# Kernel optimization log

Hardware: AMD Instinct MI355X
Metric: run time of the kernel (lower is better)

The kernel has to match this reference:

```python
import jax, jax.numpy as jnp
import numpy as np

E = 128    # embedding_size
N = 8192   # total vertices (64 graphs x 128)
CN = 512   # total color slots
G = 64     # number of graphs
TMAX = 32


def _mlp3(x, W, b):
    # 3-layer MLP: Linear-ReLU-Linear-ReLU-Linear. W: [3,E,E], b: [3,E]
    h = jax.nn.relu(x @ W[0].T + b[0])
    h = jax.nn.relu(h @ W[1].T + b[1])
    return h @ W[2].T + b[2]


def _lstm_cell(x, h, c, Wih, Whh, bih, bhh):
    # PyTorch LSTM gate order: i, f, g, o
    gates = x @ Wih.T + h @ Whh.T + (bih + bhh)
    i, f, g, o = jnp.split(gates, 4, axis=-1)
    c2 = jax.nn.sigmoid(f) * c + jax.nn.sigmoid(i) * jnp.tanh(g)
    h2 = jax.nn.sigmoid(o) * jnp.tanh(c2)
    return h2, c2


def setup_inputs() -> dict:
    key = jax.random.key(0)
    ks = jax.random.split(key, 24)
    s = 1.0 / np.sqrt(E)
    f32 = jnp.float32
    inp = {
        "M_vv": jax.random.normal(ks[0], (N, N), f32) * s,
        "M_vc": jax.random.uniform(ks[1], (N, CN), f32) * (1.0 / np.sqrt(CN)),
        "C": jax.random.normal(ks[2], (CN, E), f32),
        "slice_idx": jnp.full((G,), N // G, dtype=jnp.int32),
        "v_emb_w": jax.random.normal(ks[3], (E, 1), f32) * s,
        "v_emb_b": jax.random.normal(ks[4], (E,), f32) * s,
        "mlpC_W": jax.random.normal(ks[5], (3, E, E), f32) * s,
        "mlpC_b": jax.random.normal(ks[6], (3, E), f32) * s,
        "mlpV_W": jax.random.normal(ks[7], (3, E, E), f32) * s,
        "mlpV_b": jax.random.normal(ks[8], (3, E), f32) * s,
        "Wih_v": jax.random.normal(ks[9], (4 * E, 2 * E), f32) * s,
        "Whh_v": jax.random.normal(ks[10], (4 * E, E), f32) * s,
        "bih_v": jax.random.normal(ks[11], (4 * E,), f32) * s,
        "bhh_v": jax.random.normal(ks[12], (4 * E,), f32) * s,
        "Wih_c": jax.random.normal(ks[13], (4 * E, E), f32) * s,
        "Whh_c": jax.random.normal(ks[14], (4 * E, E), f32) * s,
        "bih_c": jax.random.normal(ks[15], (4 * E,), f32) * s,
        "bhh_c": jax.random.normal(ks[16], (4 * E,), f32) * s,
        "vote_W1": jax.random.normal(ks[17], (E, E), f32) * s,
        "vote_b1": jax.random.normal(ks[18], (E,), f32) * s,
        "vote_W2": jax.random.normal(ks[19], (E, E), f32) * s,
        "vote_b2": jax.random.normal(ks[20], (E,), f32) * s,
        "vote_W3": jax.random.normal(ks[21], (1, E), f32) * s,
        "vote_b3": jax.random.normal(ks[22], (1,), f32) * s,
    }
    return inp


def reference(M_vv, M_vc, C, slice_idx, v_emb_w, v_emb_b, mlpC_W, mlpC_b,
              mlpV_W, mlpV_b, Wih_v, Whh_v, bih_v, bhh_v, Wih_c, Whh_c,
              bih_c, bhh_c, vote_W1, vote_b1, vote_W2, vote_b2, vote_W3, vote_b3):
    n = M_vv.shape[0]
    g = slice_idx.shape[0]
    # V = v_emb(ones(1)) broadcast to all vertices: [N, E]
    v0 = v_emb_w[:, 0] + v_emb_b
    V = jnp.broadcast_to(v0, (n, E))
    # Original torch loop never reassigns V, so both LSTM inputs are
    # loop-invariant; compute them once (identical math, no recompute).
    x_v = jnp.concatenate([M_vv @ V, M_vc @ _mlp3(C, mlpC_W, mlpC_b)], axis=1)  # [N, 2E]
    x_c = M_vc.T @ _mlp3(V, mlpV_W, mlpV_b)                                      # [CN, E]

    def step(carry, _):
        hv, cv, hc, cc = carry
        hv, cv = _lstm_cell(x_v, hv, cv, Wih_v, Whh_v, bih_v, bhh_v)
        hc, cc = _lstm_cell(x_c, hc, cc, Wih_c, Whh_c, bih_c, bhh_c)
        return (hv, cv, hc, cc), None

    init = (V, jnp.zeros_like(V), C, jnp.zeros_like(C))
    (hv, cv, hc, cc), _ = jax.lax.scan(step, init, None, length=TMAX)

    # vote MLP on final vertex hidden state -> [N, 1]
    h = jax.nn.relu(hv @ vote_W1.T + vote_b1)
    h = jax.nn.relu(h @ vote_W2.T + vote_b2)
    v_vote = (h @ vote_W3.T + vote_b3)[:, 0]  # [N]

    # per-graph mean then sigmoid (torch: split + mean + sigmoid + vstack)
    seg = jnp.repeat(jnp.arange(g), slice_idx, total_repeat_length=n)
    sums = jax.ops.segment_sum(v_vote, seg, num_segments=g)
    ret = jax.nn.sigmoid(sums / slice_idx.astype(sums.dtype))
    return (ret, V[None], C)
```

## Files before the change

### kernel.cpp

```cpp
#include <hip/hip_runtime.h>
#include <hip/hip_bf16.h>
#include <stdint.h>


typedef __bf16 bf16x8 __attribute__((ext_vector_type(8)));
typedef float f32x4 __attribute__((ext_vector_type(4)));

#define EDIM 128
#define NVERT 8192
#define CNUM 512
#define NG 64
#define TSTEPS 32

#define WS_RS 0u
#define WS_V0 32768u
#define WS_W1 33280u
#define WS_BV 35328u
#define WS_ACC 37376u
#define WS_V0BF 37632u
#define WS_MLPC3T 38912u

__device__ __forceinline__ float bf2f(unsigned short s) {
  return __uint_as_float(((unsigned)s) << 16);
}
__device__ __forceinline__ unsigned short f2bf(float f) {
  unsigned u = __float_as_uint(f);
  u += 0x7fffu + ((u >> 16) & 1u);
  return (unsigned short)(u >> 16);
}
__device__ __forceinline__ float sigm(float x) {
  return __builtin_amdgcn_rcpf(1.f + __expf(-x));
}
__device__ __forceinline__ float tanh_f(float x) {
  return 1.f - 2.f * __builtin_amdgcn_rcpf(1.f + __expf(2.f * x));
}
__device__ __forceinline__ f32x4 mfma16(bf16x8 a, bf16x8 b, f32x4 c) {
  return __builtin_amdgcn_mfma_f32_16x16x32_bf16(a, b, c, 0, 0, 0);
}
__device__ __forceinline__ bf16x8 ld8(const float* p) {
  float4 a = *(const float4*)p;
  float4 b = *(const float4*)(p + 4);
  bf16x8 r;
  r[0] = (__bf16)a.x; r[1] = (__bf16)a.y; r[2] = (__bf16)a.z; r[3] = (__bf16)a.w;
  r[4] = (__bf16)b.x; r[5] = (__bf16)b.y; r[6] = (__bf16)b.z; r[7] = (__bf16)b.w;
  return r;
}

__global__ __launch_bounds__(256) void k_rowsum(
    const float* __restrict__ M, const float* __restrict__ v0,
    float* __restrict__ rs, float* __restrict__ Vout) {
  const int row = blockIdx.x;
  const float4* p = (const float4*)(M + (size_t)row * NVERT);
  float s = 0.f;
#pragma unroll
  for (int it = 0; it < 8; it++) {
    float4 q = p[it * 256 + threadIdx.x];
    s += q.x + q.y + q.z + q.w;
  }
  if (threadIdx.x < 32)
    ((float4*)(Vout + (size_t)row * EDIM))[threadIdx.x] =
        ((const float4*)v0)[threadIdx.x];
#pragma unroll
  for (int off = 32; off > 0; off >>= 1) s += __shfl_down(s, off, 64);
  __shared__ float red[4];
  if ((threadIdx.x & 63) == 0) red[threadIdx.x >> 6] = s;
  __syncthreads();
  if (threadIdx.x == 0) rs[row] = red[0] + red[1] + red[2] + red[3];
}

__global__ __launch_bounds__(512) void k_prep(
    const float* __restrict__ vw, const float* __restrict__ vb,
    const float* __restrict__ Wih,
    const float* __restrict__ bih, const float* __restrict__ bhh,
    float* __restrict__ ws) {
  __shared__ float v0s[EDIM];
  const int t = threadIdx.x;
  float* v0 = (float*)((char*)ws + WS_V0);
  float* w1 = (float*)((char*)ws + WS_W1);
  float* bv = (float*)((char*)ws + WS_BV);
  float* acc = (float*)((char*)ws + WS_ACC);
  unsigned short* v0bf = (unsigned short*)((char*)ws + WS_V0BF);
  if (t < EDIM) {
    float v = vw[t] + vb[t];
    v0s[t] = v;
    v0[t] = v;
    v0bf[t] = f2bf(v);
  }
  if (t < NG) acc[t] = 0.f;
  __syncthreads();
  {
    const float4* wr = (const float4*)(Wih + (size_t)t * 256);
    float s = 0.f;
#pragma unroll
    for (int kc = 0; kc < 32; kc++) {
      float4 q = wr[kc];
      const float* xi = v0s + kc * 4;
      s += q.x * xi[0] + q.y * xi[1] + q.z * xi[2] + q.w * xi[3];
    }
    w1[t] = s;
    bv[t] = bih[t] + bhh[t];
  }
}

__global__ __launch_bounds__(128) void k_mlpc(
    const float* __restrict__ C, const float* __restrict__ W,
    const float* __restrict__ B, float* __restrict__ ws,
    float* __restrict__ Cout) {
  unsigned short* out_t = (unsigned short*)((char*)ws + WS_MLPC3T);
  const int c = blockIdx.x, e = threadIdx.x;
  __shared__ float xb[2][EDIM];
  float cval = C[c * EDIM + e];
  xb[0][e] = cval;
  Cout[c * EDIM + e] = cval;
  __syncthreads();
#pragma unroll
  for (int l = 0; l < 3; l++) {
    const float4* wrow = (const float4*)(W + ((size_t)l * EDIM + e) * EDIM);
    const float* xin = xb[l & 1];
    float s = B[l * EDIM + e];
#pragma unroll
    for (int kc = 0; kc < EDIM / 4; kc++) {
      float4 q = wrow[kc];
      const float* xi = xin + kc * 4;
      s += q.x * xi[0] + q.y * xi[1] + q.z * xi[2] + q.w * xi[3];
    }
    if (l < 2) {
      s = fmaxf(s, 0.f);
      __syncthreads();
      xb[(l + 1) & 1][e] = s;
      __syncthreads();
    } else {
      out_t[(size_t)e * CNUM + c] = f2bf(s);
    }
  }
}

__global__ __launch_bounds__(512, 1) void k_lstm(
    const float* __restrict__ Mvc, const float* __restrict__ Wih,
    const float* __restrict__ Whh,
    const float* __restrict__ W1, const float* __restrict__ b1,
    const float* __restrict__ W2, const float* __restrict__ b2,
    const float* __restrict__ W3, const float* __restrict__ b3,
    float* __restrict__ ws) {
  const int r0 = blockIdx.x * 32;
  const int t = threadIdx.x;
  const int w = t >> 6;
  const int lane = t & 63;
  const int quad = lane >> 4;
  const int l15 = lane & 15;
  const int nc0 = w * 16;

  __shared__ unsigned short Avc[32][CNUM + 8];
  __shared__ unsigned short Tt[32][EDIM + 8];
  __shared__ unsigned short hv2[2][32][EDIM + 8];
  __shared__ float votes[32];

  const float* rs = (const float*)((const char*)ws + WS_RS);
  const float* w1v = (const float*)((const char*)ws + WS_W1);
  const float* bvv = (const float*)((const char*)ws + WS_BV);
  float* accg = (float*)((char*)ws + WS_ACC);
  const unsigned short* v0bf = (const unsigned short*)((const char*)ws + WS_V0BF);
  const unsigned short* m3t = (const unsigned short*)((const char*)ws + WS_MLPC3T);

  {
    const int row = t >> 4, c0 = t & 15;
    const float4* g = (const float4*)(Mvc + (size_t)(r0 + row) * CNUM);
#pragma unroll
    for (int it = 0; it < 8; it++) {
      int c4 = it * 16 + c0;
      float4 q = g[c4];
      ushort4 h;
      h.x = f2bf(q.x); h.y = f2bf(q.y); h.z = f2bf(q.z); h.w = f2bf(q.w);
      *(ushort4*)&Avc[row][c4 * 4] = h;
    }
  }
  for (int i = t; i < 32 * EDIM; i += 512) hv2[0][i >> 7][i & 127] = v0bf[i & 127];
  __syncthreads();

  {
    f32x4 acc[2];
#pragma unroll
    for (int mt = 0; mt < 2; mt++) {
      acc[mt][0] = 0.f; acc[mt][1] = 0.f; acc[mt][2] = 0.f; acc[mt][3] = 0.f;
    }
#pragma unroll
    for (int kc = 0; kc < 16; kc++) {
      bf16x8 a0 = *(const bf16x8*)&Avc[l15][kc * 32 + quad * 8];
      bf16x8 a1 = *(const bf16x8*)&Avc[16 + l15][kc * 32 + quad * 8];
      bf16x8 b0 = *(const bf16x8*)&m3t[(size_t)(nc0 + l15) * CNUM + kc * 32 + quad * 8];
      acc[0] = mfma16(a0, b0, acc[0]);
      acc[1] = mfma16(a1, b0, acc[1]);
    }
#pragma unroll
    for (int mt = 0; mt < 2; mt++)
#pragma unroll
      for (int r = 0; r < 4; r++)
        Tt[mt * 16 + quad * 4 + r][nc0 + l15] = f2bf(acc[mt][r]);
  }
  __syncthreads();

  f32x4 xg[2][4];
  {
    float rsv[2][4];
#pragma unroll
    for (int mt = 0; mt < 2; mt++)
#pragma unroll
      for (int r = 0; r < 4; r++) rsv[mt][r] = rs[r0 + mt * 16 + quad * 4 + r];
#pragma unroll
    for (int gi = 0; gi < 4; gi++) {
      const int col = gi * 128 + nc0 + l15;
      const float w1c = w1v[col], bvc = bvv[col];
#pragma unroll
      for (int mt = 0; mt < 2; mt++)
#pragma unroll
        for (int r = 0; r < 4; r++) xg[mt][gi][r] = fmaf(rsv[mt][r], w1c, bvc);
    }
#pragma unroll
    for (int kc = 0; kc < 4; kc++) {
      bf16x8 a0 = *(const bf16x8*)&Tt[l15][kc * 32 + quad * 8];
      bf16x8 a1 = *(const bf16x8*)&Tt[16 + l15][kc * 32 + quad * 8];
#pragma unroll
      for (int gi = 0; gi < 4; gi++) {
        const int gcol = gi * 128 + nc0 + l15;
        bf16x8 bfr = ld8(&Wih[(size_t)gcol * 256 + 128 + kc * 32 + quad * 8]);
        xg[0][gi] = mfma16(a0, bfr, xg[0][gi]);
        xg[1][gi] = mfma16(a1, bfr, xg[1][gi]);
      }
    }
  }

  bf16x8 Bh[4][4];
#pragma unroll
  for (int gi = 0; gi < 4; gi++) {
    const int gcol = gi * 128 + nc0 + l15;
#pragma unroll
    for (int kc = 0; kc < 4; kc++)
      Bh[gi][kc] = ld8(&Whh[(size_t)gcol * EDIM + kc * 32 + quad * 8]);
  }

  f32x4 cv[2];
#pragma unroll
  for (int mt = 0; mt < 2; mt++) {
    cv[mt][0] = 0.f; cv[mt][1] = 0.f; cv[mt][2] = 0.f; cv[mt][3] = 0.f;
  }

  int p = 0;
#pragma unroll 1
  for (int step = 0; step < TSTEPS; step++) {
    bf16x8 A[2][4];
#pragma unroll
    for (int mt = 0; mt < 2; mt++)
#pragma unroll
      for (int kc = 0; kc < 4; kc++)
        A[mt][kc] = *(const bf16x8*)&hv2[p][mt * 16 + l15][kc * 32 + quad * 8];
#pragma unroll
    for (int mt = 0; mt < 2; mt++) {
      f32x4 gI = xg[mt][0], gF = xg[mt][1], gG = xg[mt][2], gO = xg[mt][3];
#pragma unroll
      for (int kc = 0; kc < 4; kc++) {
        gI = mfma16(A[mt][kc], Bh[0][kc], gI);
        gF = mfma16(A[mt][kc], Bh[1][kc], gF);
        gG = mfma16(A[mt][kc], Bh[2][kc], gG);
        gO = mfma16(A[mt][kc], Bh[3][kc], gO);
      }
#pragma unroll
      for (int r = 0; r < 4; r++) {
        float ig = sigm(gI[r]), fg = sigm(gF[r]);
        float gg = tanh_f(gG[r]), og = sigm(gO[r]);
        float c2 = fmaf(fg, cv[mt][r], ig * gg);
        cv[mt][r] = c2;
        hv2[p ^ 1][mt * 16 + quad * 4 + r][nc0 + l15] = f2bf(og * tanh_f(c2));
      }
    }
    p ^= 1;
    __syncthreads();
  }

  for (int layer = 0; layer < 2; layer++) {
    const float* Wg = layer ? W2 : W1;
    const float* bg = layer ? b2 : b1;
    bf16x8 A[2][4];
#pragma unroll
    for (int mt = 0; mt < 2; mt++)
#pragma unroll
      for (int kc = 0; kc < 4; kc++)
        A[mt][kc] = *(const bf16x8*)&hv2[0][mt * 16 + l15][kc * 32 + quad * 8];
    f32x4 acc[2];
    {
      float bb = bg[nc0 + l15];
#pragma unroll
      for (int mt = 0; mt < 2; mt++) {
        acc[mt][0] = bb; acc[mt][1] = bb; acc[mt][2] = bb; acc[mt][3] = bb;
      }
    }
#pragma unroll
    for (int kc = 0; kc < 4; kc++) {
      bf16x8 bfr = ld8(&Wg[(size_t)(nc0 + l15) * EDIM + kc * 32 + quad * 8]);
      acc[0] = mfma16(A[0][kc], bfr, acc[0]);
      acc[1] = mfma16(A[1][kc], bfr, acc[1]);
    }
    __syncthreads();
#pragma unroll
    for (int mt = 0; mt < 2; mt++)
#pragma unroll
      for (int r = 0; r < 4; r++)
        hv2[0][mt * 16 + quad * 4 + r][nc0 + l15] = f2bf(fmaxf(acc[mt][r], 0.f));
    __syncthreads();
  }

  {
    const int row = t >> 4, seg = t & 15;
    float part = 0.f;
#pragma unroll
    for (int j = 0; j < 8; j++) {
      const int k = seg * 8 + j;
      part += bf2f(hv2[0][row][k]) * W3[k];
    }
    part += __shfl_down(part, 8, 16);
    part += __shfl_down(part, 4, 16);
    part += __shfl_down(part, 2, 16);
    part += __shfl_down(part, 1, 16);
    if (seg == 0) votes[row] = part + b3[0];
    __syncthreads();
    if (t < 64) {
      float v = (t < 32) ? votes[t] : 0.f;
#pragma unroll
      for (int off = 32; off > 0; off >>= 1) v += __shfl_down(v, off, 64);
      if (t == 0) atomicAdd(&accg[blockIdx.x >> 2], v);
    }
  }
}

__global__ __launch_bounds__(64) void k_final(const float* __restrict__ ws,
                                              const int* __restrict__ slice,
                                              float* __restrict__ out) {
  const float* accg = (const float*)((const char*)ws + WS_ACC);
  const int g = threadIdx.x;
  float m = accg[g] / (float)slice[g];
  out[g] = 1.f / (1.f + __expf(-m));
}

extern "C" void kernel_launch(void* const* d_in, const int* in_sizes, int n_in,
                              void* d_out, int out_size, void* d_ws, size_t ws_size,
                              hipStream_t stream) {
  const float* M_vv = (const float*)d_in[0];
  const float* M_vc = (const float*)d_in[1];
  const float* C = (const float*)d_in[2];
  const int* slice = (const int*)d_in[3];
  const float* vw = (const float*)d_in[4];
  const float* vb = (const float*)d_in[5];
  const float* mW = (const float*)d_in[6];
  const float* mB = (const float*)d_in[7];
  const float* Wih = (const float*)d_in[10];
  const float* Whh = (const float*)d_in[11];
  const float* bih = (const float*)d_in[12];
  const float* bhh = (const float*)d_in[13];
  const float* W1 = (const float*)d_in[18];
  const float* b1 = (const float*)d_in[19];
  const float* W2 = (const float*)d_in[20];
  const float* b2 = (const float*)d_in[21];
  const float* W3 = (const float*)d_in[22];
  const float* b3 = (const float*)d_in[23];
  float* ws = (float*)d_ws;
  float* out = (float*)d_out;

  k_prep<<<1, 512, 0, stream>>>(vw, vb, Wih, bih, bhh, ws);
  k_rowsum<<<NVERT, 256, 0, stream>>>(M_vv, (const float*)((char*)ws + WS_V0),
                                      (float*)((char*)ws + WS_RS), out + NG);
  k_mlpc<<<CNUM, 128, 0, stream>>>(C, mW, mB, ws, out + NG + NVERT * EDIM);
  k_lstm<<<256, 512, 0, stream>>>(M_vc, Wih, Whh, W1, b1, W2, b2, W3, b3, ws);
  k_final<<<1, 64, 0, stream>>>(ws, slice, out);
}
```

Before: 511.8 us.

## Fuse rowsum, prep and final kernels into setup and main kernels

Merges the prep kernel into the C-MLP kernel as an extra block, folds the M_vv row-sum and V output copy into the LSTM kernel, and replaces the final sigmoid kernel with a last-block-done atomic counter. This cuts the launch count from five to two and removes the separate row-sum kernel. The trade-off is that the 256MB M_vv read now runs across only 256 blocks of 512 threads at one block per CU, which may give lower memory-level parallelism than the old 8192-block row-sum kernel.

```diff
diff --git a/kernel.cpp b/kernel.cpp
--- a/kernel.cpp
+++ b/kernel.cpp
@@ -12,7 +12,7 @@
 #define NG 64
 #define TSTEPS 32
 
-#define WS_RS 0u
+#define WS_CNT 0u
 #define WS_V0 32768u
 #define WS_W1 33280u
 #define WS_BV 35328u
@@ -46,69 +46,48 @@
   return r;
 }
 
-__global__ __launch_bounds__(256) void k_rowsum(
-    const float* __restrict__ M, const float* __restrict__ v0,
-    float* __restrict__ rs, float* __restrict__ Vout) {
-  const int row = blockIdx.x;
-  const float4* p = (const float4*)(M + (size_t)row * NVERT);
-  float s = 0.f;
-#pragma unroll
-  for (int it = 0; it < 8; it++) {
-    float4 q = p[it * 256 + threadIdx.x];
-    s += q.x + q.y + q.z + q.w;
-  }
-  if (threadIdx.x < 32)
-    ((float4*)(Vout + (size_t)row * EDIM))[threadIdx.x] =
-        ((const float4*)v0)[threadIdx.x];
-#pragma unroll
-  for (int off = 32; off > 0; off >>= 1) s += __shfl_down(s, off, 64);
-  __shared__ float red[4];
-  if ((threadIdx.x & 63) == 0) red[threadIdx.x >> 6] = s;
-  __syncthreads();
-  if (threadIdx.x == 0) rs[row] = red[0] + red[1] + red[2] + red[3];
-}
-
-__global__ __launch_bounds__(512) void k_prep(
-    const float* __restrict__ vw, const float* __restrict__ vb,
-    const float* __restrict__ Wih,
+__global__ __launch_bounds__(128) void k_setup(
+    const float* __restrict__ C, const float* __restrict__ W,
+    const float* __restrict__ B, const float* __restrict__ vw,
+    const float* __restrict__ vb, const float* __restrict__ Wih,
     const float* __restrict__ bih, const float* __restrict__ bhh,
-    float* __restrict__ ws) {
-  __shared__ float v0s[EDIM];
+    float* __restrict__ ws, float* __restrict__ Cout) {
+  __shared__ float xb[2][EDIM];
   const int t = threadIdx.x;
-  float* v0 = (float*)((char*)ws + WS_V0);
-  float* w1 = (float*)((char*)ws + WS_W1);
-  float* bv = (float*)((char*)ws + WS_BV);
-  float* acc = (float*)((char*)ws + WS_ACC);
-  unsigned short* v0bf = (unsigned short*)((char*)ws + WS_V0BF);
-  if (t < EDIM) {
+
+  if (blockIdx.x == CNUM) {
+    float* v0 = (float*)((char*)ws + WS_V0);
+    float* w1 = (float*)((char*)ws + WS_W1);
+    float* bvp = (float*)((char*)ws + WS_BV);
+    float* acc = (float*)((char*)ws + WS_ACC);
+    unsigned short* v0bf = (unsigned short*)((char*)ws + WS_V0BF);
+    unsigned int* cnt = (unsigned int*)((char*)ws + WS_CNT);
     float v = vw[t] + vb[t];
-    v0s[t] = v;
+    xb[0][t] = v;
     v0[t] = v;
     v0bf[t] = f2bf(v);
-  }
-  if (t < NG) acc[t] = 0.f;
-  __syncthreads();
-  {
-    const float4* wr = (const float4*)(Wih + (size_t)t * 256);
-    float s = 0.f;
-#pragma unroll
-    for (int kc = 0; kc < 32; kc++) {
-      float4 q = wr[kc];
-      const float* xi = v0s + kc * 4;
-      s += q.x * xi[0] + q.y * xi[1] + q.z * xi[2] + q.w * xi[3];
-    }
-    w1[t] = s;
-    bv[t] = bih[t] + bhh[t];
-  }
-}
-
-__global__ __launch_bounds__(128) void k_mlpc(
-    const float* __restrict__ C, const float* __restrict__ W,
-    const float* __restrict__ B, float* __restrict__ ws,
-    float* __restrict__ Cout) {
+    if (t < NG) acc[t] = 0.f;
+    if (t == 0) *cnt = 0u;
+    __syncthreads();
+#pragma unroll
+    for (int gi = 0; gi < 4; gi++) {
+      const int col = gi * EDIM + t;
+      const float4* wr = (const float4*)(Wih + (size_t)col * 256);
+      float s = 0.f;
+#pragma unroll
+      for (int kc = 0; kc < 32; kc++) {
+        float4 q = wr[kc];
+        const float* xi = xb[0] + kc * 4;
+        s += q.x * xi[0] + q.y * xi[1] + q.z * xi[2] + q.w * xi[3];
+      }
+      w1[col] = s;
+      bvp[col] = bih[col] + bhh[col];
+    }
+    return;
+  }
+
   unsigned short* out_t = (unsigned short*)((char*)ws + WS_MLPC3T);
-  const int c = blockIdx.x, e = threadIdx.x;
-  __shared__ float xb[2][EDIM];
+  const int c = blockIdx.x, e = t;
   float cval = C[c * EDIM + e];
   xb[0][e] = cval;
   Cout[c * EDIM + e] = cval;
@@ -135,13 +114,14 @@
   }
 }
 
-__global__ __launch_bounds__(512, 1) void k_lstm(
-    const float* __restrict__ Mvc, const float* __restrict__ Wih,
-    const float* __restrict__ Whh,
+__global__ __launch_bounds__(512, 1) void k_main(
+    const float* __restrict__ Mvv, const float* __restrict__ Mvc,
+    const float* __restrict__ Wih, const float* __restrict__ Whh,
     const float* __restrict__ W1, const float* __restrict__ b1,
     const float* __restrict__ W2, const float* __restrict__ b2,
     const float* __restrict__ W3, const float* __restrict__ b3,
-    float* __restrict__ ws) {
+    const int* __restrict__ slice, float* __restrict__ ws,
+    float* __restrict__ out) {
   const int r0 = blockIdx.x * 32;
   const int t = threadIdx.x;
   const int w = t >> 6;
@@ -154,24 +134,56 @@
   __shared__ unsigned short Tt[32][EDIM + 8];
   __shared__ unsigned short hv2[2][32][EDIM + 8];
   __shared__ float votes[32];
-
-  const float* rs = (const float*)((const char*)ws + WS_RS);
+  __shared__ float rs_s[32];
+  __shared__ unsigned int last_s;
+
   const float* w1v = (const float*)((const char*)ws + WS_W1);
   const float* bvv = (const float*)((const char*)ws + WS_BV);
   float* accg = (float*)((char*)ws + WS_ACC);
+  unsigned int* cnt = (unsigned int*)((char*)ws + WS_CNT);
   const unsigned short* v0bf = (const unsigned short*)((const char*)ws + WS_V0BF);
   const unsigned short* m3t = (const unsigned short*)((const char*)ws + WS_MLPC3T);
 
   {
     const int row = t >> 4, c0 = t & 15;
     const float4* g = (const float4*)(Mvc + (size_t)(r0 + row) * CNUM);
+    float4 av[8];
+#pragma unroll
+    for (int it = 0; it < 8; it++) av[it] = g[it * 16 + c0];
+
+    const float4* mp = (const float4*)(Mvv + (size_t)(r0 + row) * NVERT) + c0;
+    float s = 0.f;
+#pragma unroll 1
+    for (int ch = 0; ch < 8; ch++) {
+      float4 q[16];
+#pragma unroll
+      for (int j = 0; j < 16; j++) q[j] = mp[ch * 256 + j * 16];
+#pragma unroll
+      for (int j = 0; j < 16; j++) s += q[j].x + q[j].y + q[j].z + q[j].w;
+    }
+    s += __shfl_down(s, 8, 16);
+    s += __shfl_down(s, 4, 16);
+    s += __shfl_down(s, 2, 16);
+    s += __shfl_down(s, 1, 16);
+    if (c0 == 0) rs_s[row] = s;
+
 #pragma unroll
     for (int it = 0; it < 8; it++) {
       int c4 = it * 16 + c0;
-      float4 q = g[c4];
       ushort4 h;
-      h.x = f2bf(q.x); h.y = f2bf(q.y); h.z = f2bf(q.z); h.w = f2bf(q.w);
+      h.x = f2bf(av[it].x); h.y = f2bf(av[it].y);
+      h.z = f2bf(av[it].z); h.w = f2bf(av[it].w);
       *(ushort4*)&Avc[row][c4 * 4] = h;
+    }
+  }
+  {
+    const float4* v04 = (const float4*)((const char*)ws + WS_V0);
+    float4* V4 = (float4*)(out + NG);
+#pragma unroll
+    for (int i = 0; i < 2; i++) {
+      int idx = t + i * 512;
+      int vr = idx >> 5, vc = idx & 31;
+      V4[(size_t)(r0 + vr) * 32 + vc] = v04[vc];
     }
   }
   for (int i = t; i < 32 * EDIM; i += 512) hv2[0][i >> 7][i & 127] = v0bf[i & 127];
@@ -205,7 +217,7 @@
 #pragma unroll
     for (int mt = 0; mt < 2; mt++)
 #pragma unroll
-      for (int r = 0; r < 4; r++) rsv[mt][r] = rs[r0 + mt * 16 + quad * 4 + r];
+      for (int r = 0; r < 4; r++) rsv[mt][r] = rs_s[mt * 16 + quad * 4 + r];
 #pragma unroll
     for (int gi = 0; gi < 4; gi++) {
       const int col = gi * 128 + nc0 + l15;
@@ -329,15 +341,21 @@
       if (t == 0) atomicAdd(&accg[blockIdx.x >> 2], v);
     }
   }
-}
-
-__global__ __launch_bounds__(64) void k_final(const float* __restrict__ ws,
-                                              const int* __restrict__ slice,
-                                              float* __restrict__ out) {
-  const float* accg = (const float*)((const char*)ws + WS_ACC);
-  const int g = threadIdx.x;
-  float m = accg[g] / (float)slice[g];
-  out[g] = 1.f / (1.f + __expf(-m));
+
+  if (t == 0) {
+    __threadfence();
+    last_s = atomicAdd(cnt, 1u);
+  }
+  __syncthreads();
+  if (last_s == 4 * NG - 1) {
+    __threadfence();
+    if (t < NG) {
+      float v = __hip_atomic_load(&accg[t], __ATOMIC_ACQUIRE,
+                                  __HIP_MEMORY_SCOPE_AGENT);
+      float m = v / (float)slice[t];
+      out[t] = 1.f / (1.f + __expf(-m));
+    }
+  }
 }
 
 extern "C" void kernel_launch(void* const* d_in, const int* in_sizes, int n_in,
@@ -364,10 +382,8 @@
   float* ws = (float*)d_ws;
   float* out = (float*)d_out;
 
-  k_prep<<<1, 512, 0, stream>>>(vw, vb, Wih, bih, bhh, ws);
-  k_rowsum<<<NVERT, 256, 0, stream>>>(M_vv, (const float*)((char*)ws + WS_V0),
-                                      (float*)((char*)ws + WS_RS), out + NG);
-  k_mlpc<<<CNUM, 128, 0, stream>>>(C, mW, mB, ws, out + NG + NVERT * EDIM);
-  k_lstm<<<256, 512, 0, stream>>>(M_vc, Wih, Whh, W1, b1, W2, b2, W3, b3, ws);
-  k_final<<<1, 64, 0, stream>>>(ws, slice, out);
-}
+  k_setup<<<CNUM + 1, 128, 0, stream>>>(C, mW, mB, vw, vb, Wih, bih, bhh, ws,
+                                        out + NG + (size_t)NVERT * EDIM);
+  k_main<<<256, 512, 0, stream>>>(M_vv, M_vc, Wih, Whh, W1, b1, W2, b2, W3, b3,
+                                  slice, ws, out);
+}
```

New measurement: 508.8 us. Within noise of the previous version (-0.6%).
